# Performance work log

Measured on AMD Instinct MI355X. Metric: run time of the kernel, lower is better.

## Reference

```python
import jax, jax.numpy as jnp
import numpy as np

N_QUBIT = 22
N_LAYERS = 2
D_LOGICAL = 2  # num_logical_dim (one logical qubit)
DIM = 2 ** N_QUBIT


def _apply_ry(psi, th, q):
    # psi: (B, 2^n) complex64; Ry(th) on qubit q (q=0 is the most significant bit)
    half = th * 0.5
    c = jnp.cos(half).astype(jnp.complex64)
    s = jnp.sin(half).astype(jnp.complex64)
    psi4 = psi.reshape(psi.shape[0], 2 ** q, 2, -1)
    p0, p1 = psi4[:, :, 0], psi4[:, :, 1]
    out = jnp.stack([c * p0 - s * p1, s * p0 + c * p1], axis=2)
    return out.reshape(psi.shape)


def _apply_cnot(psi, c, t):
    a, b = (c, t) if c < t else (t, c)
    right = 2 ** (N_QUBIT - b - 1)
    mid = 2 ** (b - a - 1)
    psi6 = psi.reshape(psi.shape[0], 2 ** a, 2, mid, 2, right)
    if c < t:
        # control is axis 2; flip target axis 4 where control==1
        psi6 = psi6.at[:, :, 1, :, :, :].set(psi6[:, :, 1, :, ::-1, :])
    else:
        # control is axis 4; flip target axis 2 where control==1
        psi6 = psi6.at[:, :, :, :, 1, :].set(psi6[:, :, ::-1, :, 1, :])
    return psi6.reshape(psi.shape)


def _apply_pauli(psi, p, q):
    psi4 = psi.reshape(psi.shape[0], 2 ** q, 2, -1)
    p0, p1 = psi4[:, :, 0], psi4[:, :, 1]
    if p == 'X':
        out = jnp.stack([p1, p0], axis=2)
    elif p == 'Y':
        out = jnp.stack([-1j * p1, 1j * p0], axis=2)
    else:  # Z
        out = jnp.stack([p0, -p1], axis=2)
    return out.reshape(psi.shape)


def _encode(theta):
    # q0[i, i] = 1 for the logical basis states, then run the circuit
    psi = jnp.zeros((D_LOGICAL, DIM), jnp.complex64)
    psi = psi.at[jnp.arange(D_LOGICAL), jnp.arange(D_LOGICAL)].set(1.0)
    for l in range(N_LAYERS):
        for q in range(N_QUBIT):
            psi = _apply_ry(psi, theta[l, q], q)
        for q in range(N_QUBIT):
            psi = _apply_cnot(psi, q, (q + 1) % N_QUBIT)
    return psi


def _kl_loss(theta):
    psi = _encode(theta)  # (D_LOGICAL, 2^n)
    # Knill-Laflamme inner products T_e[i,j] = <psi_i| E_e |psi_j> for all weight-1 Paulis
    Ts = []
    for q in range(N_QUBIT):
        for p in ('X', 'Y', 'Z'):
            epsi = _apply_pauli(psi, p, q)
            Ts.append(jnp.einsum('is,js->ij', psi.conj(), epsi))
    T = jnp.stack(Ts)  # (3*N_QUBIT, D_LOGICAL, D_LOGICAL)
    diag = jnp.diagonal(T, axis1=1, axis2=2)
    lam = diag.mean(axis=1)  # per-error lambda_e
    res = T - lam[:, None, None] * jnp.eye(D_LOGICAL, dtype=T.dtype)
    # loss_type == 'L2'
    return jnp.sum(jnp.abs(res) ** 2)


def setup_inputs() -> dict:
    key = jax.random.key(0)
    theta = jax.random.normal(key, (N_LAYERS, N_QUBIT), dtype=jnp.float32)
    return {"theta": theta}


def reference(theta):
    return _kl_loss(theta)
```

## Files before the change

kernel.cpp:

```cpp
#include <hip/hip_runtime.h>

#define NQ 22
#define DIMN (1u << NQ)

struct MaskSet {
    unsigned L[NQ];
    unsigned Linv[NQ];
    unsigned xm[NQ];
    unsigned zm[NQ];
    unsigned frowHi[5];
};

constexpr MaskSet buildMasks() {
    MaskSet M{};
    for (int b = 0; b < NQ; ++b) M.L[b] = 1u << b;
    for (int q = 0; q < NQ; ++q) {
        int bc = NQ - 1 - q, bt = NQ - 1 - ((q + 1) % NQ);
        M.L[bt] ^= M.L[bc];
    }
    unsigned mat[NQ] = {}, aug[NQ] = {};
    for (int b = 0; b < NQ; ++b) { mat[b] = M.L[b]; aug[b] = 1u << b; }
    for (int col = 0; col < NQ; ++col) {
        int piv = col;
        while (!((mat[piv] >> col) & 1u)) ++piv;
        unsigned tm = mat[piv]; mat[piv] = mat[col]; mat[col] = tm;
        unsigned ta = aug[piv]; aug[piv] = aug[col]; aug[col] = ta;
        for (int r = 0; r < NQ; ++r)
            if (r != col && ((mat[r] >> col) & 1u)) { mat[r] ^= mat[col]; aug[r] ^= aug[col]; }
    }
    for (int b = 0; b < NQ; ++b) M.Linv[b] = aug[b];
    for (int j = 0; j < NQ; ++j) {
        int b = NQ - 1 - j;
        unsigned xmv = 0;
        for (int r = 0; r < NQ; ++r)
            if ((aug[r] >> b) & 1u) xmv |= 1u << r;
        M.xm[j] = xmv;
        M.zm[j] = M.L[b];
    }
    for (int j = 0; j < 5; ++j) {
        unsigned f = 0;
        for (int r = 0; r < NQ; ++r)
            if ((aug[r] >> (17 + j)) & 1u) f |= 1u << r;
        M.frowHi[j] = f;
    }
    return M;
}
constexpr int topbit_c(unsigned v) { int b = 0; while (v >> (b + 1)) ++b; return b; }
constexpr unsigned unionHi() {
    MaskSet M = buildMasks();
    unsigned u = 0;
    for (int j = 0; j < 5; ++j) u |= M.frowHi[j];
    return u;
}
static_assert((unionHi() & 0xFFFFu) == 0, "frowHi must only touch bits 16..21");

__device__ __forceinline__ float wave_sum(float v) {
    v += __shfl_down(v, 32); v += __shfl_down(v, 16); v += __shfl_down(v, 8);
    v += __shfl_down(v, 4);  v += __shfl_down(v, 2);  v += __shfl_down(v, 1);
    return v;
}
__device__ __forceinline__ float fflip(float v, unsigned sbit31) {
    return __int_as_float(__float_as_int(v) ^ (int)sbit31);
}
__device__ __forceinline__ unsigned ph4(unsigned g) { return g ^ ((g >> 6) & 3u); }

__global__ __launch_bounds__(256) void k_prep(const float* __restrict__ theta,
                                              float* __restrict__ acc,
                                              float* __restrict__ trig) {
    int t = threadIdx.x;
    acc[t] = 0.f;
    if (t < 2 * NQ) {
        int l = t / NQ, q = t % NQ, b = NQ - 1 - q;
        float h = 0.5f * theta[t];
        trig[l * 2 * NQ + b]      = cosf(h);
        trig[l * 2 * NQ + NQ + b] = sinf(h);
    }
}

__global__ __launch_bounds__(256, 1) void k_genHi(float* __restrict__ phi,
                                                  const float* __restrict__ trig,
                                                  float* __restrict__ acc) {
    constexpr MaskSet M = buildMasks();
    __shared__ float red[4 * 12];
    unsigned base = blockIdx.x * 256u + threadIdx.x;
    unsigned P0 = 0;
#pragma unroll
    for (int b = 0; b < NQ; ++b)
        P0 |= ((unsigned)__popc(base & M.Linv[b]) & 1u) << b;
    float pc = 1.f;
#pragma unroll
    for (int b = 1; b < 16; ++b) {
        float cvb = trig[b], svb = trig[NQ + b];
        pc *= ((P0 >> b) & 1u) ? svb : cvb;
    }
    float cv0 = trig[0], sv0 = trig[NQ];
    float C0 = pc * ((P0 & 1u) ? sv0 : cv0);
    float C1 = pc * ((P0 & 1u) ? cv0 : -sv0);
    float cb[6], sb[6];
#pragma unroll
    for (int k = 0; k < 6; ++k) { cb[k] = trig[16 + k]; sb[k] = trig[NQ + 16 + k]; }
    unsigned u0 = P0 >> 16;
    float v0[32], v1[32];
#pragma unroll
    for (int e = 0; e < 32; ++e) {
        unsigned F = 0;
        if (e & 1)  F ^= M.frowHi[0];
        if (e & 2)  F ^= M.frowHi[1];
        if (e & 4)  F ^= M.frowHi[2];
        if (e & 8)  F ^= M.frowHi[3];
        if (e & 16) F ^= M.frowHi[4];
        unsigned u = u0 ^ (F >> 16);
        float vp = (u & 1u) ? sb[0] : cb[0];
#pragma unroll
        for (int k = 1; k < 6; ++k) vp *= ((u >> k) & 1u) ? sb[k] : cb[k];
        v0[e] = vp * C0;
        v1[e] = vp * C1;
    }
    float c2[5], s2[5];
#pragma unroll
    for (int j = 0; j < 5; ++j) {
        c2[j] = trig[2 * NQ + 17 + j];
        s2[j] = trig[3 * NQ + 17 + j];
    }
#pragma unroll
    for (int j = 0; j < 5; ++j) {
#pragma unroll
        for (int e = 0; e < 32; ++e) {
            if (!(e & (1 << j))) {
                int e1 = e | (1 << j);
                float a0 = v0[e], a1 = v0[e1];
                v0[e]  = c2[j] * a0 - s2[j] * a1;
                v0[e1] = s2[j] * a0 + c2[j] * a1;
                float b0 = v1[e], b1 = v1[e1];
                v1[e]  = c2[j] * b0 - s2[j] * b1;
                v1[e1] = s2[j] * b0 + c2[j] * b1;
            }
        }
    }
#pragma unroll
    for (int e = 0; e < 32; ++e) {
        unsigned a = base | ((unsigned)e << 17);
        phi[a] = v0[e];
        phi[DIMN + a] = v1[e];
    }
    int lane = threadIdx.x & 63, w = threadIdx.x >> 6;
#pragma unroll
    for (int i = 1; i <= 3; ++i) {
        unsigned ex  = M.xm[i] >> 17;
        unsigned zme = M.zm[i] >> 17;
        float t00 = 0.f, t11 = 0.f, t01 = 0.f, u01 = 0.f;
#pragma unroll
        for (int e = 0; e < 32; ++e) {
            int ep = e ^ (int)ex;
            t00 += v0[e] * v0[ep];
            t11 += v1[e] * v1[ep];
            float p = v0[e] * v1[ep];
            t01 += p;
            unsigned sg = ((unsigned)__popc((unsigned)ep & zme) & 1u) << 31;
            u01 += fflip(p, sg);
        }
        float vals[4] = { t00, t11, t01, u01 };
#pragma unroll
        for (int j = 0; j < 4; ++j) {
            float v = wave_sum(vals[j]);
            if (lane == 0) red[w * 12 + (i - 1) * 4 + j] = v;
        }
    }
    __syncthreads();
    int t = threadIdx.x;
    if (t < 12) {
        float r = red[t] + red[12 + t] + red[24 + t] + red[36 + t];
        atomicAdd(&acc[4 + t], r);
    }
}

__global__ __launch_bounds__(256, 1) void k_midA(float* __restrict__ phi,
                                                 const float* __restrict__ trig,
                                                 float* __restrict__ acc) {
    constexpr MaskSet M = buildMasks();
    __shared__ float red[4 * 16];
    unsigned tid = blockIdx.x * 256u + threadIdx.x;
    unsigned base = (tid & 0xFFFu) | ((tid >> 12) << 17);
    float v0[32], v1[32];
#pragma unroll
    for (int e = 0; e < 32; ++e) {
        unsigned a = base | ((unsigned)e << 12);
        v0[e] = phi[a];
        v1[e] = phi[DIMN + a];
    }
    float c[5], s[5];
#pragma unroll
    for (int j = 0; j < 5; ++j) {
        c[j] = trig[2 * NQ + 12 + j];
        s[j] = trig[3 * NQ + 12 + j];
    }
#pragma unroll
    for (int j = 0; j < 5; ++j) {
#pragma unroll
        for (int e = 0; e < 32; ++e) {
            if (!(e & (1 << j))) {
                int e1 = e | (1 << j);
                float a0 = v0[e], a1 = v0[e1];
                v0[e]  = c[j] * a0 - s[j] * a1;
                v0[e1] = s[j] * a0 + c[j] * a1;
                float b0 = v1[e], b1 = v1[e1];
                v1[e]  = c[j] * b0 - s[j] * b1;
                v1[e1] = s[j] * b0 + c[j] * b1;
            }
        }
    }
#pragma unroll
    for (int e = 0; e < 32; ++e) {
        unsigned a = base | ((unsigned)e << 12);
        phi[a] = v0[e];
        phi[DIMN + a] = v1[e];
    }
    int lane = threadIdx.x & 63, w = threadIdx.x >> 6;
#pragma unroll
    for (int i = 5; i <= 8; ++i) {
        unsigned ex  = (M.xm[i] >> 12) & 31u;
        unsigned zme = (M.zm[i] >> 12) & 31u;
        unsigned bs31 = ((unsigned)__popc(base & M.zm[i]) & 1u) << 31;
        float t00 = 0.f, t11 = 0.f, t01 = 0.f, u01 = 0.f;
#pragma unroll
        for (int e = 0; e < 32; ++e) {
            int ep = e ^ (int)ex;
            t00 += v0[e] * v0[ep];
            t11 += v1[e] * v1[ep];
            float p = v0[e] * v1[ep];
            t01 += p;
            unsigned sg = ((unsigned)__popc((unsigned)ep & zme) & 1u) << 31;
            u01 += fflip(p, sg ^ bs31);
        }
        float vals[4] = { t00, t11, t01, u01 };
#pragma unroll
        for (int j = 0; j < 4; ++j) {
            float v = wave_sum(vals[j]);
            if (lane == 0) red[w * 16 + (i - 5) * 4 + j] = v;
        }
    }
    __syncthreads();
    int t = threadIdx.x;
    if (t < 16) {
        float r = red[t] + red[16 + t] + red[32 + t] + red[48 + t];
        atomicAdd(&acc[20 + t], r);
    }
}

__global__ __launch_bounds__(256) void k_low(float* __restrict__ phi,
                                             const float* __restrict__ trig,
                                             float* __restrict__ acc) {
    constexpr MaskSet M = buildMasks();
    __shared__ float As[4096];
    __shared__ float Bs[4096];
    __shared__ float red[4 * 44];
    float4* As4 = (float4*)As;
    float4* Bs4 = (float4*)Bs;
    int t = threadIdx.x;
    unsigned base = blockIdx.x * 4096u;
    float a[16], b[16];

    {
        const float4* g0 = (const float4*)(phi + base);
        const float4* g1 = (const float4*)(phi + DIMN + base);
#pragma unroll
        for (int k = 0; k < 4; ++k) {
            float4 va = g0[4 * t + k];
            a[4 * k] = va.x; a[4 * k + 1] = va.y; a[4 * k + 2] = va.z; a[4 * k + 3] = va.w;
            float4 vb = g1[4 * t + k];
            b[4 * k] = vb.x; b[4 * k + 1] = vb.y; b[4 * k + 2] = vb.z; b[4 * k + 3] = vb.w;
        }
#pragma unroll
        for (int g = 0; g < 4; ++g) {
            float c = trig[2 * NQ + g], s = trig[3 * NQ + g];
#pragma unroll
            for (int e = 0; e < 16; ++e) {
                if (!(e & (1 << g))) {
                    int e1 = e | (1 << g);
                    float x0 = a[e], x1 = a[e1];
                    a[e] = c * x0 - s * x1; a[e1] = s * x0 + c * x1;
                    float y0 = b[e], y1 = b[e1];
                    b[e] = c * y0 - s * y1; b[e1] = s * y0 + c * y1;
                }
            }
        }
        unsigned sw = (unsigned)(t >> 4) & 3u;
#pragma unroll
        for (int k = 0; k < 4; ++k) {
            unsigned f = ((unsigned)(4 * t + k)) ^ sw;
            As4[f] = make_float4(a[4 * k], a[4 * k + 1], a[4 * k + 2], a[4 * k + 3]);
            Bs4[f] = make_float4(b[4 * k], b[4 * k + 1], b[4 * k + 2], b[4 * k + 3]);
        }
    }
    __syncthreads();

    {
        unsigned lo = (unsigned)t & 15u, hi = (unsigned)t >> 4;
        unsigned swz = (hi & 3u) << 2;
#pragma unroll
        for (int j = 0; j < 16; ++j) {
            unsigned i = lo | ((unsigned)j << 4) | (hi << 8);
            a[j] = As[i ^ swz];
            b[j] = Bs[i ^ swz];
        }
#pragma unroll
        for (int g = 0; g < 4; ++g) {
            float c = trig[2 * NQ + 4 + g], s = trig[3 * NQ + 4 + g];
#pragma unroll
            for (int e = 0; e < 16; ++e) {
                if (!(e & (1 << g))) {
                    int e1 = e | (1 << g);
                    float x0 = a[e], x1 = a[e1];
                    a[e] = c * x0 - s * x1; a[e1] = s * x0 + c * x1;
                    float y0 = b[e], y1 = b[e1];
                    b[e] = c * y0 - s * y1; b[e1] = s * y0 + c * y1;
                }
            }
        }
#pragma unroll
        for (int j = 0; j < 16; ++j) {
            unsigned i = lo | ((unsigned)j << 4) | (hi << 8);
            As[i ^ swz] = a[j];
            Bs[i ^ swz] = b[j];
        }
    }
    __syncthreads();

    {
#pragma unroll
        for (int j = 0; j < 16; ++j) {
            unsigned i = (unsigned)t | ((unsigned)j << 8);
            unsigned p = i ^ (((unsigned)j & 3u) << 2);
            a[j] = As[p];
            b[j] = Bs[p];
        }
#pragma unroll
        for (int g = 0; g < 4; ++g) {
            float c = trig[2 * NQ + 8 + g], s = trig[3 * NQ + 8 + g];
#pragma unroll
            for (int e = 0; e < 16; ++e) {
                if (!(e & (1 << g))) {
                    int e1 = e | (1 << g);
                    float x0 = a[e], x1 = a[e1];
                    a[e] = c * x0 - s * x1; a[e1] = s * x0 + c * x1;
                    float y0 = b[e], y1 = b[e1];
                    b[e] = c * y0 - s * y1; b[e1] = s * y0 + c * y1;
                }
            }
        }
#pragma unroll
        for (int j = 0; j < 16; ++j) {
            unsigned i = (unsigned)t | ((unsigned)j << 8);
            phi[base + i] = a[j];
            phi[DIMN + base + i] = b[j];
            unsigned p = i ^ (((unsigned)j & 3u) << 2);
            As[p] = a[j];
            Bs[p] = b[j];
        }
    }

    float SSv[3], z0v[3], z1v[3], z2v[3], d4v[3];
    {
#pragma unroll
        for (int c = 0; c < 3; ++c) {
            float p[16];
#pragma unroll
            for (int j = 0; j < 16; ++j)
                p[j] = (c == 0) ? a[j] * a[j] : (c == 1) ? b[j] * b[j] : a[j] * b[j];
            float s1[8], d1[8];
#pragma unroll
            for (int j = 0; j < 8; ++j) { s1[j] = p[j] + p[j + 8]; d1[j] = p[j] - p[j + 8]; }
            float s2[4], d2[4];
#pragma unroll
            for (int j = 0; j < 4; ++j) { s2[j] = s1[j] + s1[j + 4]; d2[j] = d1[j] - d1[j + 4]; }
            float d3a = d2[0] - d2[2], d3b = d2[1] - d2[3];
            SSv[c] = (s2[0] + s2[1]) + (s2[2] + s2[3]);
            z0v[c] = ((d1[0] + d1[1]) + (d1[2] + d1[3])) + ((d1[4] + d1[5]) + (d1[6] + d1[7]));
            z1v[c] = (d2[0] + d2[1]) + (d2[2] + d2[3]);
            z2v[c] = d3a + d3b;
            d4v[c] = d3a - d3b;
        }
    }
    {
        unsigned Wt = (unsigned)t;
        Wt ^= Wt >> 1; Wt ^= Wt >> 2; Wt ^= Wt >> 4;
        int lane = t & 63, w = t >> 6;
#pragma unroll
        for (int c = 0; c < 3; ++c) {
            float v;
            v = wave_sum(SSv[c]); if (lane == 0) red[w * 39 + c] = v;
            v = wave_sum(z0v[c]); if (lane == 0) red[w * 39 + 3 + c] = v;
            v = wave_sum(z1v[c]); if (lane == 0) red[w * 39 + 6 + c] = v;
            v = wave_sum(z2v[c]); if (lane == 0) red[w * 39 + 9 + c] = v;
            v = wave_sum(d4v[c]); if (lane == 0) red[w * 39 + 12 + c] = v;
#pragma unroll
            for (int k = 4; k < 12; ++k) {
                unsigned sb = ((Wt >> (11 - k)) & 1u) << 31;
                v = wave_sum(fflip(d4v[c], sb));
                if (lane == 0) red[w * 39 + 3 + 3 * k + c] = v;
            }
        }
    }
    __syncthreads();
    if (t < 66) {
        int c = t % 3, q = t / 3;
        int slot = (q == 0 || q == 21) ? (3 + 33 + c) : (q < 10 ? c : 3 + 3 * (q - 10) + c);
        float val = red[slot] + red[39 + slot] + red[78 + slot] + red[117 + slot];
        unsigned sg = (unsigned)__popc(base & M.zm[q]) & 1u;
        atomicAdd(&acc[4 * NQ + 3 * q + c], sg ? -val : val);
    }
    __syncthreads();

    int lane = t & 63, w = t >> 6;

#pragma unroll
    for (int i = 0; i < 3; ++i) {
        constexpr int qn0 = 10;
        unsigned je  = (M.xm[qn0 + i] >> 8) & 15u;
        unsigned zmj = (M.zm[qn0 + i] >> 8) & 15u;
        unsigned zb31 = ((unsigned)__popc(base & M.zm[qn0 + i]) & 1u) << 31;
        float t00 = 0.f, t11 = 0.f, t01 = 0.f, u01 = 0.f;
#pragma unroll
        for (int j = 0; j < 16; ++j) {
            int jp = j ^ (int)je;
            t00 += a[j] * a[jp];
            t11 += b[j] * b[jp];
            float p = a[j] * b[jp];
            t01 += p;
            unsigned sg = ((unsigned)__popc((unsigned)jp & zmj) & 1u) << 31;
            u01 += fflip(p, sg ^ zb31);
        }
        float vals[4] = { t00, t11, t01, u01 };
#pragma unroll
        for (int j = 0; j < 4; ++j) {
            float v = wave_sum(vals[j]);
            if (lane == 0) red[w * 44 + 4 * i + j] = v;
        }
    }

#pragma unroll
    for (int i = 3; i < 11; ++i) {
        unsigned m = M.xm[10 + i], zm = M.zm[10 + i];
        unsigned zb = (unsigned)__popc(base & zm) & 1u;
        float t00 = 0.f, t11 = 0.f, t01 = 0.f, u01 = 0.f;
        if (i < 10) {
            int gb = topbit_c(M.xm[10 + i]) - 2;
            unsigned mg4 = m >> 2;
            unsigned swap2 = m & 3u;
#pragma unroll
            for (int r = 0; r < 2; ++r) {
                unsigned gc = (unsigned)t + 256u * r;
                unsigned g = ((gc >> gb) << (gb + 1)) | (gc & ((1u << gb) - 1u));
                unsigned gx = g ^ mg4;
                float4 a0 = As4[ph4(g)],  a1 = Bs4[ph4(g)];
                float4 b0 = As4[ph4(gx)], b1 = Bs4[ph4(gx)];
                if (swap2) {
                    b0 = make_float4(b0.z, b0.w, b0.x, b0.y);
                    b1 = make_float4(b1.z, b1.w, b1.x, b1.y);
                }
                unsigned szg = ((unsigned)__popc((g << 2) & zm) + zb) & 1u;
                unsigned szx = ((unsigned)__popc((gx << 2) & zm) + zb) & 1u;
                unsigned fg = szg << 31, fx = szx << 31;
                const float* A0 = &a0.x; const float* A1 = &a1.x;
                const float* B0 = &b0.x; const float* B1 = &b1.x;
#pragma unroll
                for (int j = 0; j < 4; ++j) {
                    t00 += A0[j] * B0[j];
                    t11 += A1[j] * B1[j];
                    float p = A0[j] * B1[j], r2 = B0[j] * A1[j];
                    t01 += p + r2;
                    u01 += fflip(p, fx) + fflip(r2, fg);
                }
            }
            t00 *= 2.f; t11 *= 2.f;
        } else {
#pragma unroll
            for (int k = 0; k < 4; ++k) {
                unsigned g = (unsigned)t + 256u * k;
                float4 a0 = As4[ph4(g)], a1 = Bs4[ph4(g)];
                unsigned szg = ((unsigned)__popc((g << 2) & zm) + zb) & 1u;
                const float* A0 = &a0.x; const float* A1 = &a1.x;
#pragma unroll
                for (int j = 0; j < 4; ++j) {
                    int jx = j ^ 3;
                    float p = A0[j] * A0[jx];
                    float q2 = A1[j] * A1[jx];
                    float cr = A0[j] * A1[jx];
                    t00 += p; t11 += q2; t01 += cr;
                    unsigned sj = ((unsigned)(jx >> 1) & 1u) ^ szg;
                    u01 += fflip(cr, sj << 31);
                }
            }
        }
        float vals[4] = { t00, t11, t01, u01 };
#pragma unroll
        for (int j = 0; j < 4; ++j) {
            float v = wave_sum(vals[j]);
            if (lane == 0) red[w * 44 + 4 * i + j] = v;
        }
    }
    __syncthreads();
    if (t < 44) {
        float r = red[t] + red[44 + t] + red[88 + t] + red[132 + t];
        atomicAdd(&acc[40 + t], r);
    }
}

struct Meas4Arg { unsigned xm[4]; unsigned zm[4]; int gbit[4]; int qn[4]; };

__global__ __launch_bounds__(256) void k_measS(const float* __restrict__ phi,
                                               float* __restrict__ acc,
                                               Meas4Arg M) {
    __shared__ float red[16];
    int t = threadIdx.x;
    int slice = blockIdx.y;
    unsigned m = M.xm[slice], zm = M.zm[slice];
    int gb = M.gbit[slice];
    unsigned mg4 = m >> 2;
    unsigned ml2 = m & 3u;
    unsigned zl = zm & 3u;
    unsigned pg31[4], px31[4];
#pragma unroll
    for (int j = 0; j < 4; ++j) {
        pg31[j] = (((unsigned)__popc((unsigned)j & zl) & 1u) << 31);
        px31[j] = (((unsigned)__popc(((unsigned)j ^ ml2) & zl) & 1u) << 31);
    }
    unsigned tid = blockIdx.x * 256u + (unsigned)t;
    const float4* p0 = (const float4*)phi;
    const float4* p1 = (const float4*)(phi + DIMN);
    float t00 = 0.f, t11 = 0.f, t01 = 0.f, u01 = 0.f;
#pragma unroll
    for (int it = 0; it < 8; ++it) {
        unsigned gc = tid + (unsigned)it * 65536u;
        unsigned g = ((gc >> gb) << (gb + 1)) | (gc & ((1u << gb) - 1u));
        unsigned gx = g ^ mg4;
        float4 a0 = p0[g], a1 = p1[g];
        float4 b0 = p0[gx], b1 = p1[gx];
        if (ml2) {
            b0 = make_float4(b0.y, b0.x, b0.w, b0.z);
            b1 = make_float4(b1.y, b1.x, b1.w, b1.z);
        }
        unsigned fg = (((unsigned)__popc((g << 2) & zm) & 1u) << 31);
        unsigned fx = (((unsigned)__popc((gx << 2) & zm) & 1u) << 31);
        const float* A0 = &a0.x; const float* A1 = &a1.x;
        const float* B0 = &b0.x; const float* B1 = &b1.x;
#pragma unroll
        for (int j = 0; j < 4; ++j) {
            t00 += A0[j] * B0[j];
            t11 += A1[j] * B1[j];
            float p = A0[j] * B1[j], r = B0[j] * A1[j];
            t01 += p + r;
            u01 += fflip(p, fx ^ px31[j]) + fflip(r, fg ^ pg31[j]);
        }
    }
    t00 *= 2.f; t11 *= 2.f;
    int lane = t & 63, w = t >> 6;
    float vals[4] = { t00, t11, t01, u01 };
#pragma unroll
    for (int j = 0; j < 4; ++j) {
        float v = wave_sum(vals[j]);
        if (lane == 0) red[w * 4 + j] = v;
    }
    __syncthreads();
    if (t < 4) {
        float r = red[t] + red[4 + t] + red[8 + t] + red[12 + t];
        atomicAdd(&acc[4 * M.qn[slice] + t], r);
    }
}

__global__ __launch_bounds__(64) void k_final(const float* __restrict__ acc,
                                              float* __restrict__ out) {
    int t = threadIdx.x;
    float v = 0.f;
    if (t < NQ) {
        float t00 = acc[4 * t], t11 = acc[4 * t + 1];
        float t01 = acc[4 * t + 2], u01 = acc[4 * t + 3];
        float d = t00 - t11;
        v = 0.5f * d * d + 2.f * t01 * t01 + 2.f * u01 * u01;
    } else if (t < 2 * NQ) {
        int q = t - NQ;
        float z0 = acc[4 * NQ + 3 * q], z1 = acc[4 * NQ + 3 * q + 1];
        float zz = acc[4 * NQ + 3 * q + 2];
        float d = z0 - z1;
        v = 0.5f * d * d + 2.f * zz * zz;
    }
    v += __shfl_down(v, 32); v += __shfl_down(v, 16); v += __shfl_down(v, 8);
    v += __shfl_down(v, 4);  v += __shfl_down(v, 2);  v += __shfl_down(v, 1);
    if (t == 0) out[0] = v;
}

extern "C" void kernel_launch(void* const* d_in, const int* in_sizes, int n_in,
                              void* d_out, int out_size, void* d_ws, size_t ws_size,
                              hipStream_t stream) {
    const float* theta = (const float*)d_in[0];
    float* out  = (float*)d_out;
    float* ws   = (float*)d_ws;
    float* phi  = ws;
    float* acc  = ws + 2 * (size_t)DIMN;
    float* trig = acc + 256;

    constexpr MaskSet M = buildMasks();

    Meas4Arg m4;
    const int qs[4] = { 0, 4, 9, 21 };
    for (int i = 0; i < 4; ++i) {
        int q = qs[i];
        m4.xm[i] = M.xm[q]; m4.zm[i] = M.zm[q];
        m4.gbit[i] = topbit_c(M.xm[q]) - 2;
        m4.qn[i] = q;
    }

    k_prep<<<1, 256, 0, stream>>>(theta, acc, trig);
    k_genHi<<<512, 256, 0, stream>>>(phi, trig, acc);
    k_midA<<<512, 256, 0, stream>>>(phi, trig, acc);
    k_low<<<1024, 256, 0, stream>>>(phi, trig, acc);
    k_measS<<<dim3(256, 4), 256, 0, stream>>>(phi, acc, m4);
    k_final<<<1, 64, 0, stream>>>(acc, out);
}
```

Measured before the change: 165.0 us.

## Restructure k_low to 512 threads with 8 amplitudes per thread in four radix-8 passes

k_low now runs 512 threads per block, each holding 8 amplitudes per state instead of 16. The 12 low-qubit rotations are applied in four 3-qubit passes through shared memory, with new swizzle patterns. The Z and X/Y measurement reductions are rewritten for the new thread-to-index mapping, including a shuffle-based butterfly for parity sums. The aim is lower register pressure and more waves per CU to hide memory latency, at the cost of an extra barrier and shared-memory round trip plus more cross-wave reduction work.

```diff
diff --git a/kernel.cpp b/kernel.cpp
--- a/kernel.cpp
+++ b/kernel.cpp
@@ -62,7 +62,8 @@
 __device__ __forceinline__ float fflip(float v, unsigned sbit31) {
     return __int_as_float(__float_as_int(v) ^ (int)sbit31);
 }
-__device__ __forceinline__ unsigned ph4(unsigned g) { return g ^ ((g >> 6) & 3u); }
+__device__ __forceinline__ unsigned psw(unsigned i)  { return i ^ (((i >> 6) & 7u) << 3); }
+__device__ __forceinline__ unsigned pg4(unsigned g)  { return g ^ (((g >> 4) & 7u) << 1); }
 
 __global__ __launch_bounds__(256) void k_prep(const float* __restrict__ theta,
                                               float* __restrict__ acc,
@@ -247,34 +248,37 @@
     }
 }
 
-__global__ __launch_bounds__(256) void k_low(float* __restrict__ phi,
-                                             const float* __restrict__ trig,
-                                             float* __restrict__ acc) {
+__global__ __launch_bounds__(512, 4) void k_low(float* __restrict__ phi,
+                                                const float* __restrict__ trig,
+                                                float* __restrict__ acc) {
     constexpr MaskSet M = buildMasks();
     __shared__ float As[4096];
     __shared__ float Bs[4096];
-    __shared__ float red[4 * 44];
+    __shared__ float red[384];
     float4* As4 = (float4*)As;
     float4* Bs4 = (float4*)Bs;
     int t = threadIdx.x;
+    int lane = t & 63, w = t >> 6;
     unsigned base = blockIdx.x * 4096u;
-    float a[16], b[16];
+    float a[8], b[8];
+    unsigned sz1 = (((unsigned)t >> 3) & 7u) << 3;
+    unsigned sz3 = (((unsigned)t >> 6) & 7u) << 3;
 
     {
         const float4* g0 = (const float4*)(phi + base);
         const float4* g1 = (const float4*)(phi + DIMN + base);
 #pragma unroll
-        for (int k = 0; k < 4; ++k) {
-            float4 va = g0[4 * t + k];
-            a[4 * k] = va.x; a[4 * k + 1] = va.y; a[4 * k + 2] = va.z; a[4 * k + 3] = va.w;
-            float4 vb = g1[4 * t + k];
-            b[4 * k] = vb.x; b[4 * k + 1] = vb.y; b[4 * k + 2] = vb.z; b[4 * k + 3] = vb.w;
-        }
-#pragma unroll
-        for (int g = 0; g < 4; ++g) {
+        for (int h = 0; h < 2; ++h) {
+            float4 va = g0[2 * t + h];
+            a[4 * h] = va.x; a[4 * h + 1] = va.y; a[4 * h + 2] = va.z; a[4 * h + 3] = va.w;
+            float4 vb = g1[2 * t + h];
+            b[4 * h] = vb.x; b[4 * h + 1] = vb.y; b[4 * h + 2] = vb.z; b[4 * h + 3] = vb.w;
+        }
+#pragma unroll
+        for (int g = 0; g < 3; ++g) {
             float c = trig[2 * NQ + g], s = trig[3 * NQ + g];
 #pragma unroll
-            for (int e = 0; e < 16; ++e) {
+            for (int e = 0; e < 8; ++e) {
                 if (!(e & (1 << g))) {
                     int e1 = e | (1 << g);
                     float x0 = a[e], x1 = a[e1];
@@ -284,30 +288,27 @@
                 }
             }
         }
-        unsigned sw = (unsigned)(t >> 4) & 3u;
-#pragma unroll
-        for (int k = 0; k < 4; ++k) {
-            unsigned f = ((unsigned)(4 * t + k)) ^ sw;
-            As4[f] = make_float4(a[4 * k], a[4 * k + 1], a[4 * k + 2], a[4 * k + 3]);
-            Bs4[f] = make_float4(b[4 * k], b[4 * k + 1], b[4 * k + 2], b[4 * k + 3]);
+#pragma unroll
+        for (int h = 0; h < 2; ++h) {
+            unsigned f4 = (2u * t + h) ^ (sz1 >> 2);
+            As4[f4] = make_float4(a[4 * h], a[4 * h + 1], a[4 * h + 2], a[4 * h + 3]);
+            Bs4[f4] = make_float4(b[4 * h], b[4 * h + 1], b[4 * h + 2], b[4 * h + 3]);
         }
     }
     __syncthreads();
 
     {
-        unsigned lo = (unsigned)t & 15u, hi = (unsigned)t >> 4;
-        unsigned swz = (hi & 3u) << 2;
-#pragma unroll
-        for (int j = 0; j < 16; ++j) {
-            unsigned i = lo | ((unsigned)j << 4) | (hi << 8);
-            a[j] = As[i ^ swz];
-            b[j] = Bs[i ^ swz];
-        }
-#pragma unroll
-        for (int g = 0; g < 4; ++g) {
-            float c = trig[2 * NQ + 4 + g], s = trig[3 * NQ + 4 + g];
-#pragma unroll
-            for (int e = 0; e < 16; ++e) {
+#pragma unroll
+        for (int k = 0; k < 8; ++k) {
+            unsigned i = ((unsigned)t & 7u) | ((unsigned)k << 3) | (((unsigned)t >> 3) << 6);
+            a[k] = As[i ^ sz1];
+            b[k] = Bs[i ^ sz1];
+        }
+#pragma unroll
+        for (int g = 0; g < 3; ++g) {
+            float c = trig[2 * NQ + 3 + g], s = trig[3 * NQ + 3 + g];
+#pragma unroll
+            for (int e = 0; e < 8; ++e) {
                 if (!(e & (1 << g))) {
                     int e1 = e | (1 << g);
                     float x0 = a[e], x1 = a[e1];
@@ -318,27 +319,27 @@
             }
         }
 #pragma unroll
-        for (int j = 0; j < 16; ++j) {
-            unsigned i = lo | ((unsigned)j << 4) | (hi << 8);
-            As[i ^ swz] = a[j];
-            Bs[i ^ swz] = b[j];
+        for (int k = 0; k < 8; ++k) {
+            unsigned i = ((unsigned)t & 7u) | ((unsigned)k << 3) | (((unsigned)t >> 3) << 6);
+            As[i ^ sz1] = a[k];
+            Bs[i ^ sz1] = b[k];
         }
     }
     __syncthreads();
 
     {
 #pragma unroll
-        for (int j = 0; j < 16; ++j) {
-            unsigned i = (unsigned)t | ((unsigned)j << 8);
-            unsigned p = i ^ (((unsigned)j & 3u) << 2);
-            a[j] = As[p];
-            b[j] = Bs[p];
-        }
-#pragma unroll
-        for (int g = 0; g < 4; ++g) {
-            float c = trig[2 * NQ + 8 + g], s = trig[3 * NQ + 8 + g];
-#pragma unroll
-            for (int e = 0; e < 16; ++e) {
+        for (int k = 0; k < 8; ++k) {
+            unsigned i = ((unsigned)t & 63u) | ((unsigned)k << 6) | (((unsigned)t >> 6) << 9);
+            unsigned p = i ^ ((unsigned)k << 3);
+            a[k] = As[p];
+            b[k] = Bs[p];
+        }
+#pragma unroll
+        for (int g = 0; g < 3; ++g) {
+            float c = trig[2 * NQ + 6 + g], s = trig[3 * NQ + 6 + g];
+#pragma unroll
+            for (int e = 0; e < 8; ++e) {
                 if (!(e & (1 << g))) {
                     int e1 = e | (1 << g);
                     float x0 = a[e], x1 = a[e1];
@@ -349,87 +350,168 @@
             }
         }
 #pragma unroll
-        for (int j = 0; j < 16; ++j) {
-            unsigned i = (unsigned)t | ((unsigned)j << 8);
-            phi[base + i] = a[j];
-            phi[DIMN + base + i] = b[j];
-            unsigned p = i ^ (((unsigned)j & 3u) << 2);
-            As[p] = a[j];
-            Bs[p] = b[j];
-        }
-    }
-
-    float SSv[3], z0v[3], z1v[3], z2v[3], d4v[3];
+        for (int k = 0; k < 8; ++k) {
+            unsigned i = ((unsigned)t & 63u) | ((unsigned)k << 6) | (((unsigned)t >> 6) << 9);
+            unsigned p = i ^ ((unsigned)k << 3);
+            As[p] = a[k];
+            Bs[p] = b[k];
+        }
+    }
+    __syncthreads();
+
     {
 #pragma unroll
-        for (int c = 0; c < 3; ++c) {
-            float p[16];
-#pragma unroll
-            for (int j = 0; j < 16; ++j)
-                p[j] = (c == 0) ? a[j] * a[j] : (c == 1) ? b[j] * b[j] : a[j] * b[j];
-            float s1[8], d1[8];
-#pragma unroll
-            for (int j = 0; j < 8; ++j) { s1[j] = p[j] + p[j + 8]; d1[j] = p[j] - p[j + 8]; }
-            float s2[4], d2[4];
-#pragma unroll
-            for (int j = 0; j < 4; ++j) { s2[j] = s1[j] + s1[j + 4]; d2[j] = d1[j] - d1[j + 4]; }
-            float d3a = d2[0] - d2[2], d3b = d2[1] - d2[3];
-            SSv[c] = (s2[0] + s2[1]) + (s2[2] + s2[3]);
-            z0v[c] = ((d1[0] + d1[1]) + (d1[2] + d1[3])) + ((d1[4] + d1[5]) + (d1[6] + d1[7]));
-            z1v[c] = (d2[0] + d2[1]) + (d2[2] + d2[3]);
-            z2v[c] = d3a + d3b;
-            d4v[c] = d3a - d3b;
-        }
-    }
-    {
-        unsigned Wt = (unsigned)t;
-        Wt ^= Wt >> 1; Wt ^= Wt >> 2; Wt ^= Wt >> 4;
-        int lane = t & 63, w = t >> 6;
-#pragma unroll
-        for (int c = 0; c < 3; ++c) {
-            float v;
-            v = wave_sum(SSv[c]); if (lane == 0) red[w * 39 + c] = v;
-            v = wave_sum(z0v[c]); if (lane == 0) red[w * 39 + 3 + c] = v;
-            v = wave_sum(z1v[c]); if (lane == 0) red[w * 39 + 6 + c] = v;
-            v = wave_sum(z2v[c]); if (lane == 0) red[w * 39 + 9 + c] = v;
-            v = wave_sum(d4v[c]); if (lane == 0) red[w * 39 + 12 + c] = v;
-#pragma unroll
-            for (int k = 4; k < 12; ++k) {
-                unsigned sb = ((Wt >> (11 - k)) & 1u) << 31;
-                v = wave_sum(fflip(d4v[c], sb));
-                if (lane == 0) red[w * 39 + 3 + 3 * k + c] = v;
-            }
+        for (int k = 0; k < 8; ++k) {
+            unsigned i = (unsigned)t | ((unsigned)k << 9);
+            a[k] = As[i ^ sz3];
+            b[k] = Bs[i ^ sz3];
+        }
+#pragma unroll
+        for (int g = 0; g < 3; ++g) {
+            float c = trig[2 * NQ + 9 + g], s = trig[3 * NQ + 9 + g];
+#pragma unroll
+            for (int e = 0; e < 8; ++e) {
+                if (!(e & (1 << g))) {
+                    int e1 = e | (1 << g);
+                    float x0 = a[e], x1 = a[e1];
+                    a[e] = c * x0 - s * x1; a[e1] = s * x0 + c * x1;
+                    float y0 = b[e], y1 = b[e1];
+                    b[e] = c * y0 - s * y1; b[e1] = s * y0 + c * y1;
+                }
+            }
+        }
+#pragma unroll
+        for (int k = 0; k < 8; ++k) {
+            unsigned i = (unsigned)t | ((unsigned)k << 9);
+            phi[base + i] = a[k];
+            phi[DIMN + base + i] = b[k];
+            As[i ^ sz3] = a[k];
+            Bs[i ^ sz3] = b[k];
+        }
+    }
+
+#pragma unroll
+    for (int c = 0; c < 3; ++c) {
+        float p[8];
+#pragma unroll
+        for (int j = 0; j < 8; ++j)
+            p[j] = (c == 0) ? a[j] * a[j] : (c == 1) ? b[j] * b[j] : a[j] * b[j];
+        float a1[4], b1[4];
+#pragma unroll
+        for (int j = 0; j < 4; ++j) { a1[j] = p[j] + p[j + 4]; b1[j] = p[j] - p[j + 4]; }
+        float a2[2], b2[2];
+#pragma unroll
+        for (int j = 0; j < 2; ++j) { a2[j] = a1[j] + a1[j + 2]; b2[j] = b1[j] - b1[j + 2]; }
+        float SS  = a2[0] + a2[1];
+        float T11 = (b1[0] + b1[1]) + (b1[2] + b1[3]);
+        float T10 = b2[0] + b2[1];
+        float T9  = b2[0] - b2[1];
+        float v;
+        v = wave_sum(SS);  if (lane == 0) red[w * 30 + c * 10 + 0] = v;
+        v = wave_sum(T9);  if (lane == 0) red[w * 30 + c * 10 + 1] = v;
+        v = wave_sum(T10); if (lane == 0) red[w * 30 + c * 10 + 2] = v;
+        v = wave_sum(T11); if (lane == 0) red[w * 30 + c * 10 + 3] = v;
+        float u = T9;
+#pragma unroll
+        for (int bl = 5; bl >= 0; --bl) {
+            u = u - __shfl_xor(u, 1 << bl);
+            float f = u;
+#pragma unroll
+            for (int bb = bl - 1; bb >= 0; --bb) f += __shfl_xor(f, 1 << bb);
+            if (lane == 0) red[w * 30 + c * 10 + 4 + bl] = f;
         }
     }
     __syncthreads();
     if (t < 66) {
         int c = t % 3, q = t / 3;
-        int slot = (q == 0 || q == 21) ? (3 + 33 + c) : (q < 10 ? c : 3 + 3 * (q - 10) + c);
-        float val = red[slot] + red[39 + slot] + red[78 + slot] + red[117 + slot];
-        unsigned sg = (unsigned)__popc(base & M.zm[q]) & 1u;
-        atomicAdd(&acc[4 * NQ + 3 * q + c], sg ? -val : val);
-    }
-    __syncthreads();
-
-    int lane = t & 63, w = t >> 6;
-
-#pragma unroll
-    for (int i = 0; i < 3; ++i) {
-        constexpr int qn0 = 10;
-        unsigned je  = (M.xm[qn0 + i] >> 8) & 15u;
-        unsigned zmj = (M.zm[qn0 + i] >> 8) & 15u;
-        unsigned zb31 = ((unsigned)__popc(base & M.zm[qn0 + i]) & 1u) << 31;
+        unsigned bs = (unsigned)__popc(base & M.zm[q]) & 1u;
+        float val = 0.f;
+        if (q >= 1 && q <= 9) {
+#pragma unroll
+            for (int w2 = 0; w2 < 8; ++w2) val += red[w2 * 30 + c * 10 + 0];
+        } else if (q >= 10 && q <= 12) {
+            int slot = (q == 10) ? 3 : (q == 11) ? 2 : 1;
+#pragma unroll
+            for (int w2 = 0; w2 < 8; ++w2) val += red[w2 * 30 + c * 10 + slot];
+        } else if (q >= 13 && q <= 15) {
+#pragma unroll
+            for (int w2 = 0; w2 < 8; ++w2) {
+                unsigned sg = (q == 13) ? ((unsigned)(w2 >> 2) & 1u)
+                            : (q == 14) ? ((((unsigned)w2 >> 1) ^ ((unsigned)w2 >> 2)) & 1u)
+                                        : ((unsigned)__popc((unsigned)w2) & 1u);
+                float r = red[w2 * 30 + c * 10 + 1];
+                val += sg ? -r : r;
+            }
+        } else {
+            int m = (q == 0) ? 0 : 21 - q;
+#pragma unroll
+            for (int w2 = 0; w2 < 8; ++w2) {
+                unsigned sg = (unsigned)__popc((unsigned)w2) & 1u;
+                float r = red[w2 * 30 + c * 10 + 4 + m];
+                val += sg ? -r : r;
+            }
+        }
+        atomicAdd(&acc[4 * NQ + 3 * q + c], bs ? -val : val);
+    }
+    __syncthreads();
+
+#pragma unroll
+    for (int qi = 10; qi <= 11; ++qi) {
+        unsigned exk = (M.xm[qi] >> 9) & 7u;
+        unsigned zmk = (M.zm[qi] >> 9) & 7u;
+        unsigned zb31 = ((unsigned)__popc(base & M.zm[qi]) & 1u) << 31;
         float t00 = 0.f, t11 = 0.f, t01 = 0.f, u01 = 0.f;
 #pragma unroll
-        for (int j = 0; j < 16; ++j) {
-            int jp = j ^ (int)je;
-            t00 += a[j] * a[jp];
-            t11 += b[j] * b[jp];
-            float p = a[j] * b[jp];
+        for (int k = 0; k < 8; ++k) {
+            int kp = k ^ (int)exk;
+            t00 += a[k] * a[kp];
+            t11 += b[k] * b[kp];
+            float p = a[k] * b[kp];
             t01 += p;
-            unsigned sg = ((unsigned)__popc((unsigned)jp & zmj) & 1u) << 31;
+            unsigned sg = ((unsigned)__popc((unsigned)kp & zmk) & 1u) << 31;
             u01 += fflip(p, sg ^ zb31);
         }
+        float vals[4] = { t00, t11, t01, u01 };
+#pragma unroll
+        for (int j = 0; j < 4; ++j) {
+            float v = wave_sum(vals[j]);
+            if (lane == 0) red[w * 44 + (qi - 10) * 4 + j] = v;
+        }
+    }
+
+#pragma unroll
+    for (int i = 2; i < 10; ++i) {
+        unsigned m = M.xm[10 + i], zm = M.zm[10 + i];
+        unsigned zb = (unsigned)__popc(base & zm) & 1u;
+        int gb = topbit_c(M.xm[10 + i]) - 2;
+        unsigned mg4 = m >> 2;
+        unsigned swap2 = m & 3u;
+        float t00 = 0.f, t11 = 0.f, t01 = 0.f, u01 = 0.f;
+        {
+            unsigned gc = (unsigned)t;
+            unsigned g = ((gc >> gb) << (gb + 1)) | (gc & ((1u << gb) - 1u));
+            unsigned gx = g ^ mg4;
+            float4 a0 = As4[pg4(g)],  a1 = Bs4[pg4(g)];
+            float4 b0 = As4[pg4(gx)], b1 = Bs4[pg4(gx)];
+            if (swap2) {
+                b0 = make_float4(b0.z, b0.w, b0.x, b0.y);
+                b1 = make_float4(b1.z, b1.w, b1.x, b1.y);
+            }
+            unsigned szg = ((unsigned)__popc((g << 2) & zm) + zb) & 1u;
+            unsigned szx = ((unsigned)__popc((gx << 2) & zm) + zb) & 1u;
+            unsigned fg = szg << 31, fx = szx << 31;
+            const float* A0 = &a0.x; const float* A1 = &a1.x;
+            const float* B0 = &b0.x; const float* B1 = &b1.x;
+#pragma unroll
+            for (int j = 0; j < 4; ++j) {
+                t00 += A0[j] * B0[j];
+                t11 += A1[j] * B1[j];
+                float p = A0[j] * B1[j], r2 = B0[j] * A1[j];
+                t01 += p + r2;
+                u01 += fflip(p, fx) + fflip(r2, fg);
+            }
+        }
+        t00 *= 2.f; t11 *= 2.f;
         float vals[4] = { t00, t11, t01, u01 };
 #pragma unroll
         for (int j = 0; j < 4; ++j) {
@@ -438,70 +520,39 @@
         }
     }
 
-#pragma unroll
-    for (int i = 3; i < 11; ++i) {
-        unsigned m = M.xm[10 + i], zm = M.zm[10 + i];
+    {
+        unsigned zm = M.zm[20];
         unsigned zb = (unsigned)__popc(base & zm) & 1u;
         float t00 = 0.f, t11 = 0.f, t01 = 0.f, u01 = 0.f;
-        if (i < 10) {
-            int gb = topbit_c(M.xm[10 + i]) - 2;
-            unsigned mg4 = m >> 2;
-            unsigned swap2 = m & 3u;
-#pragma unroll
-            for (int r = 0; r < 2; ++r) {
-                unsigned gc = (unsigned)t + 256u * r;
-                unsigned g = ((gc >> gb) << (gb + 1)) | (gc & ((1u << gb) - 1u));
-                unsigned gx = g ^ mg4;
-                float4 a0 = As4[ph4(g)],  a1 = Bs4[ph4(g)];
-                float4 b0 = As4[ph4(gx)], b1 = Bs4[ph4(gx)];
-                if (swap2) {
-                    b0 = make_float4(b0.z, b0.w, b0.x, b0.y);
-                    b1 = make_float4(b1.z, b1.w, b1.x, b1.y);
-                }
-                unsigned szg = ((unsigned)__popc((g << 2) & zm) + zb) & 1u;
-                unsigned szx = ((unsigned)__popc((gx << 2) & zm) + zb) & 1u;
-                unsigned fg = szg << 31, fx = szx << 31;
-                const float* A0 = &a0.x; const float* A1 = &a1.x;
-                const float* B0 = &b0.x; const float* B1 = &b1.x;
-#pragma unroll
-                for (int j = 0; j < 4; ++j) {
-                    t00 += A0[j] * B0[j];
-                    t11 += A1[j] * B1[j];
-                    float p = A0[j] * B1[j], r2 = B0[j] * A1[j];
-                    t01 += p + r2;
-                    u01 += fflip(p, fx) + fflip(r2, fg);
-                }
-            }
-            t00 *= 2.f; t11 *= 2.f;
-        } else {
-#pragma unroll
-            for (int k = 0; k < 4; ++k) {
-                unsigned g = (unsigned)t + 256u * k;
-                float4 a0 = As4[ph4(g)], a1 = Bs4[ph4(g)];
-                unsigned szg = ((unsigned)__popc((g << 2) & zm) + zb) & 1u;
-                const float* A0 = &a0.x; const float* A1 = &a1.x;
-#pragma unroll
-                for (int j = 0; j < 4; ++j) {
-                    int jx = j ^ 3;
-                    float p = A0[j] * A0[jx];
-                    float q2 = A1[j] * A1[jx];
-                    float cr = A0[j] * A1[jx];
-                    t00 += p; t11 += q2; t01 += cr;
-                    unsigned sj = ((unsigned)(jx >> 1) & 1u) ^ szg;
-                    u01 += fflip(cr, sj << 31);
-                }
+#pragma unroll
+        for (int k2 = 0; k2 < 2; ++k2) {
+            unsigned g = (unsigned)t + 512u * k2;
+            float4 a0 = As4[pg4(g)], a1 = Bs4[pg4(g)];
+            unsigned szg = ((unsigned)__popc((g << 2) & zm) + zb) & 1u;
+            const float* A0 = &a0.x; const float* A1 = &a1.x;
+#pragma unroll
+            for (int j = 0; j < 4; ++j) {
+                int jx = j ^ 3;
+                float p = A0[j] * A0[jx];
+                float q2 = A1[j] * A1[jx];
+                float cr = A0[j] * A1[jx];
+                t00 += p; t11 += q2; t01 += cr;
+                unsigned sj = ((unsigned)(jx >> 1) & 1u) ^ szg;
+                u01 += fflip(cr, sj << 31);
             }
         }
         float vals[4] = { t00, t11, t01, u01 };
 #pragma unroll
         for (int j = 0; j < 4; ++j) {
             float v = wave_sum(vals[j]);
-            if (lane == 0) red[w * 44 + 4 * i + j] = v;
+            if (lane == 0) red[w * 44 + 40 + j] = v;
         }
     }
     __syncthreads();
     if (t < 44) {
-        float r = red[t] + red[44 + t] + red[88 + t] + red[132 + t];
+        float r = 0.f;
+#pragma unroll
+        for (int w2 = 0; w2 < 8; ++w2) r += red[w2 * 44 + t];
         atomicAdd(&acc[40 + t], r);
     }
 }
@@ -613,7 +664,7 @@
     k_prep<<<1, 256, 0, stream>>>(theta, acc, trig);
     k_genHi<<<512, 256, 0, stream>>>(phi, trig, acc);
     k_midA<<<512, 256, 0, stream>>>(phi, trig, acc);
-    k_low<<<1024, 256, 0, stream>>>(phi, trig, acc);
+    k_low<<<1024, 512, 0, stream>>>(phi, trig, acc);
     k_measS<<<dim3(256, 4), 256, 0, stream>>>(phi, acc, m4);
     k_final<<<1, 64, 0, stream>>>(acc, out);
 }
```

After: 168.5 us. +2.1%, slower.
